# Kernel optimization log

Hardware: AMD Instinct MI355X
Metric: run time of the kernel (lower is better)

## Reference

```python
import jax, jax.numpy as jnp
import numpy as np

M_GROUP = 8  # VENOM m: pattern period along in_features

def _nm_mask(in_features, dtype):
    # NMVectorSparsifier.get_random_mask keeps positions 0 and 2 of every group of m=8
    pat = jnp.array([1.0, 0.0, 1.0, 0.0, 0.0, 0.0, 0.0, 0.0], dtype=dtype)
    return jnp.tile(pat, in_features // M_GROUP)  # [in_features]


def setup_inputs() -> dict:
    key = jax.random.key(0)
    k1, k2, k3 = jax.random.split(key, 3)
    B, S, D_IN, D_OUT = 8, 2048, 4096, 4096
    x = jax.random.normal(k1, (B, S, D_IN), dtype=jnp.float32)
    weight = jax.random.normal(k2, (D_OUT, D_IN), dtype=jnp.float32) * 0.02
    bias = jax.random.normal(k3, (D_OUT,), dtype=jnp.float32) * 0.02
    return {"x": x, "weight": weight, "bias": bias}


def reference(x, weight, bias):
    # y = x @ (W * mask)^T + b  -- N:M (2:8) vector-sparse linear, dense-math reference
    mask = _nm_mask(weight.shape[1], weight.dtype)  # [D_IN]
    w = weight * mask[None, :]                      # [D_OUT, D_IN]
    return jnp.einsum('bsd,od->bso', x, w) + bias
```

## Files before the change

### kernel.cpp

```cpp
#include <hip/hip_runtime.h>
#include <hip/hip_bf16.h>
#include <stdint.h>

#define MROWS 16384
#define DIN   4096
#define DOUT  4096
#define KEFF  1024

typedef __attribute__((ext_vector_type(8))) __bf16 bf16x8;
typedef __attribute__((ext_vector_type(4))) float f32x4;

#define AS1 __attribute__((address_space(1)))
#define AS3 __attribute__((address_space(3)))

__device__ __forceinline__ uint32_t f2bf_rne(float f) {
  union { float f; uint32_t u; } v; v.f = f;
  uint32_t u = v.u;
  return (u + 0x7fffu + ((u >> 16) & 1u)) >> 16;
}

__global__ void venom_gather_all(const float* __restrict__ x,
                                 const float* __restrict__ w,
                                 uint2* __restrict__ xg, uint2* __restrict__ wg) {
  const int PX = MROWS * (DIN / 16);
  const int PW = DOUT * (DIN / 16);
  int stride = gridDim.x * blockDim.x;
  for (int i = blockIdx.x * blockDim.x + threadIdx.x; i < PX + PW; i += stride) {
    const float* src; uint2* dst; int idx;
    if (i < PX) { src = x; dst = xg; idx = i; }
    else        { src = w; dst = wg; idx = i - PX; }
    const float4* p = reinterpret_cast<const float4*>(src) + (size_t)idx * 4;
    float4 a = p[0];
    float4 b = p[2];
    uint2 r;
    r.x = f2bf_rne(a.x) | (f2bf_rne(a.z) << 16);
    r.y = f2bf_rne(b.x) | (f2bf_rne(b.z) << 16);
    dst[idx] = r;
  }
}

#define BM 256
#define BN 256
#define BK 64
#define NT (KEFF / BK)
#define TPB 4
#define LTOT (NT * TPB)

__device__ __forceinline__ int swz_off(int R, int lg) {
  int sr = R >> 1;
  return sr * 128 + (((((R & 1) << 2) | lg) ^ (sr & 7)) << 4);
}

#define WAIT_VM(n) asm volatile("s_waitcnt vmcnt(" #n ")" ::: "memory")
#define BAR() __builtin_amdgcn_s_barrier()

__global__ __launch_bounds__(512, 2) void venom_gemm_p3(
    const __bf16* __restrict__ A, const __bf16* __restrict__ Bm,
    const float* __restrict__ bias, float* __restrict__ C) {
  __shared__ __bf16 As[2][2][128 * 64];
  __shared__ __bf16 Bs[2][2][128 * 64];

  int nwg = gridDim.x;
  int cpx = nwg >> 3;
  int bid = blockIdx.x;
  int swz = (bid & 7) * cpx + (bid >> 3);
  int mblk = swz >> 2;
  int ngrp = swz & 3;

  int t = threadIdx.x;
  int wid = t >> 6, l = t & 63;
  int wr = wid >> 2, wc = wid & 3;
  int lr = l & 15, lg = l >> 4;

  const __bf16* Ag = A + (size_t)(mblk * BM) * KEFF;

  float biasr[TPB][4];
  #pragma unroll
  for (int j = 0; j < TPB; ++j)
    #pragma unroll
    for (int ni = 0; ni < 4; ++ni)
      biasr[j][ni] = bias[(ngrp * TPB + j) * BN + wc * 64 + ni * 16 + lr];

  f32x4 acc[8][4] = {};

  auto stage_half = [&](int L2, int kh) {
    const int buf = L2 & 1;
    const int j2 = L2 >> 4;
    const int kt2 = L2 & (NT - 1);
    const __bf16* Bg = Bm + (size_t)((ngrp * TPB + j2) * BN) * KEFF;
    const int k0 = kt2 * BK + kh * 32;
    #pragma unroll
    for (int i = 0; i < 2; ++i) {
      int e = i * 512 + t;
      int sr = e >> 3;
      int s = (e & 7) ^ (sr & 7);
      int row = sr * 2 + (s >> 2);
      int koff = (s & 3) * 8;
      __builtin_amdgcn_global_load_lds(
          (const AS1 uint32_t*)(Ag + (size_t)row * KEFF + k0 + koff),
          ((AS3 uint32_t*)&As[buf][kh][0]) + e * 4, 16, 0, 0);
      __builtin_amdgcn_global_load_lds(
          (const AS1 uint32_t*)(Bg + (size_t)row * KEFF + k0 + koff),
          ((AS3 uint32_t*)&Bs[buf][kh][0]) + e * 4, 16, 0, 0);
    }
  };

  stage_half(0, 0);
  stage_half(0, 1);
  stage_half(1, 0);
  WAIT_VM(8);
  BAR();

  bf16x8 bfrag[4];

  #pragma unroll
  for (int j = 0; j < TPB; ++j) {
    #pragma unroll 1
    for (int kt = 0; kt < NT; ++kt) {
      const int L = j * NT + kt;
      const int cur = kt & 1;

      #pragma unroll
      for (int ph = 0; ph < 4; ++ph) {
        const int mh = ph & 1, kh = ph >> 1;
        const char* aB = (const char*)&As[cur][kh][0];
        bf16x8 af[4];
        #pragma unroll
        for (int mi = 0; mi < 4; ++mi)
          af[mi] = *(const bf16x8*)(aB + swz_off(wr * 128 + mh * 64 + mi * 16 + lr, lg));
        if (mh == 0) {
          const char* bB = (const char*)&Bs[cur][kh][0];
          #pragma unroll
          for (int ni = 0; ni < 4; ++ni)
            bfrag[ni] = *(const bf16x8*)(bB + swz_off(wc * 64 + ni * 16 + lr, lg));
          if (kh == 0) { if (L + 1 < LTOT) stage_half(L + 1, 1); }
          else         { if (L + 2 < LTOT) stage_half(L + 2, 0); }
        }

        BAR();
        __builtin_amdgcn_s_setprio(1);
        #pragma unroll
        for (int mi = 0; mi < 4; ++mi)
          #pragma unroll
          for (int ni = 0; ni < 4; ++ni)
            acc[mh * 4 + mi][ni] = __builtin_amdgcn_mfma_f32_16x16x32_bf16(
                af[mi], bfrag[ni], acc[mh * 4 + mi][ni], 0, 0, 0);
        __builtin_amdgcn_s_setprio(0);

        if (ph == 1) {
          if (L <= LTOT - 2) WAIT_VM(8);
          else               WAIT_VM(0);
          BAR();
        } else if (ph == 3) {
          if (L <= LTOT - 3)      WAIT_VM(8);
          else if (L == LTOT - 2) WAIT_VM(4);
          else                    WAIT_VM(0);
          BAR();
        } else {
          BAR();
        }
      }
    }

    {
      int colbase = (ngrp * TPB + j) * BN + wc * 64;
      int rowbase = mblk * BM + wr * 128;
      #pragma unroll
      for (int mh = 0; mh < 2; ++mh)
        #pragma unroll
        for (int mi = 0; mi < 4; ++mi) {
          int row0 = rowbase + mh * 64 + mi * 16 + lg * 4;
          #pragma unroll
          for (int ni = 0; ni < 4; ++ni) {
            int col = colbase + ni * 16 + lr;
            f32x4 cv = acc[mh * 4 + mi][ni];
            #pragma unroll
            for (int jj = 0; jj < 4; ++jj)
              C[(size_t)(row0 + jj) * DOUT + col] = cv[jj] + biasr[j][ni];
          }
        }
      #pragma unroll
      for (int q = 0; q < 8; ++q)
        #pragma unroll
        for (int ni = 0; ni < 4; ++ni)
          acc[q][ni] = (f32x4){0.f, 0.f, 0.f, 0.f};
    }
  }
}

__global__ void venom_naive(const float* __restrict__ x, const float* __restrict__ w,
                            const float* __restrict__ bias, float* __restrict__ out) {
  size_t total = (size_t)MROWS * DOUT;
  size_t stride = (size_t)gridDim.x * blockDim.x;
  for (size_t idx = (size_t)blockIdx.x * blockDim.x + threadIdx.x; idx < total;
       idx += stride) {
    int m = (int)(idx / DOUT), n = (int)(idx % DOUT);
    const float* xr = x + (size_t)m * DIN;
    const float* wr = w + (size_t)n * DIN;
    float s = 0.f;
    for (int g = 0; g < DIN / 8; ++g)
      s += xr[g * 8] * wr[g * 8] + xr[g * 8 + 2] * wr[g * 8 + 2];
    out[idx] = s + bias[n];
  }
}

extern "C" void kernel_launch(void* const* d_in, const int* in_sizes, int n_in,
                              void* d_out, int out_size, void* d_ws, size_t ws_size,
                              hipStream_t stream) {
  const float* x    = (const float*)d_in[0];
  const float* wgt  = (const float*)d_in[1];
  const float* bias = (const float*)d_in[2];
  float* out = (float*)d_out;

  const size_t xg_bytes = (size_t)MROWS * KEFF * 2;
  const size_t wg_bytes = (size_t)DOUT * KEFF * 2;

  if (ws_size < xg_bytes + wg_bytes) {
    venom_naive<<<2048, 256, 0, stream>>>(x, wgt, bias, out);
    return;
  }

  uint32_t* xg = (uint32_t*)d_ws;
  uint32_t* wg = (uint32_t*)((char*)d_ws + xg_bytes);

  venom_gather_all<<<2048, 256, 0, stream>>>(x, wgt, (uint2*)xg, (uint2*)wg);

  venom_gemm_p3<<<(MROWS / BM) * (DOUT / BN / TPB), 512, 0, stream>>>(
      (const __bf16*)xg, (const __bf16*)wg, bias, out);
}
```

Before: 287.0 us.

## Switch GEMM to 32x32x16 MFMA tiles and restructure prefetch pipeline

New measurement: 293.3 us. 1.02x slower.

```diff
diff --git a/kernel.cpp b/kernel.cpp
--- a/kernel.cpp
+++ b/kernel.cpp
@@ -7,8 +7,8 @@
 #define DOUT  4096
 #define KEFF  1024
 
-typedef __attribute__((ext_vector_type(8))) __bf16 bf16x8;
-typedef __attribute__((ext_vector_type(4))) float f32x4;
+typedef __attribute__((ext_vector_type(8)))  __bf16 bf16x8;
+typedef __attribute__((ext_vector_type(16))) float  f32x16;
 
 #define AS1 __attribute__((address_space(1)))
 #define AS3 __attribute__((address_space(3)))
@@ -46,15 +46,15 @@
 #define TPB 4
 #define LTOT (NT * TPB)
 
-__device__ __forceinline__ int swz_off(int R, int lg) {
+__device__ __forceinline__ int swz_off(int R, int slot) {
   int sr = R >> 1;
-  return sr * 128 + (((((R & 1) << 2) | lg) ^ (sr & 7)) << 4);
+  return sr * 128 + (((((R & 1) << 2) | slot) ^ (sr & 7)) << 4);
 }
 
 #define WAIT_VM(n) asm volatile("s_waitcnt vmcnt(" #n ")" ::: "memory")
 #define BAR() __builtin_amdgcn_s_barrier()
 
-__global__ __launch_bounds__(512, 2) void venom_gemm_p3(
+__global__ __launch_bounds__(512, 2) void venom_gemm_w32(
     const __bf16* __restrict__ A, const __bf16* __restrict__ Bm,
     const float* __restrict__ bias, float* __restrict__ C) {
   __shared__ __bf16 As[2][2][128 * 64];
@@ -70,25 +70,22 @@
   int t = threadIdx.x;
   int wid = t >> 6, l = t & 63;
   int wr = wid >> 2, wc = wid & 3;
-  int lr = l & 15, lg = l >> 4;
+  int lc = l & 31, hi = l >> 5;
 
   const __bf16* Ag = A + (size_t)(mblk * BM) * KEFF;
 
-  float biasr[TPB][4];
+  float biasr[TPB][2];
   #pragma unroll
   for (int j = 0; j < TPB; ++j)
     #pragma unroll
-    for (int ni = 0; ni < 4; ++ni)
-      biasr[j][ni] = bias[(ngrp * TPB + j) * BN + wc * 64 + ni * 16 + lr];
-
-  f32x4 acc[8][4] = {};
-
-  auto stage_half = [&](int L2, int kh) {
+    for (int tj = 0; tj < 2; ++tj)
+      biasr[j][tj] = bias[(ngrp * TPB + j) * BN + wc * 64 + tj * 32 + lc];
+
+  f32x16 acc[4][2] = {};
+
+  auto stageA = [&](int L2, int kh) {
     const int buf = L2 & 1;
-    const int j2 = L2 >> 4;
-    const int kt2 = L2 & (NT - 1);
-    const __bf16* Bg = Bm + (size_t)((ngrp * TPB + j2) * BN) * KEFF;
-    const int k0 = kt2 * BK + kh * 32;
+    const int k0 = (L2 & (NT - 1)) * BK + kh * 32;
     #pragma unroll
     for (int i = 0; i < 2; ++i) {
       int e = i * 512 + t;
@@ -99,19 +96,31 @@
       __builtin_amdgcn_global_load_lds(
           (const AS1 uint32_t*)(Ag + (size_t)row * KEFF + k0 + koff),
           ((AS3 uint32_t*)&As[buf][kh][0]) + e * 4, 16, 0, 0);
+    }
+  };
+  auto stageB = [&](int L2, int kh) {
+    const int buf = L2 & 1;
+    const __bf16* Bg = Bm + (size_t)((ngrp * TPB + (L2 >> 4)) * BN) * KEFF;
+    const int k0 = (L2 & (NT - 1)) * BK + kh * 32;
+    #pragma unroll
+    for (int i = 0; i < 2; ++i) {
+      int e = i * 512 + t;
+      int sr = e >> 3;
+      int s = (e & 7) ^ (sr & 7);
+      int row = sr * 2 + (s >> 2);
+      int koff = (s & 3) * 8;
       __builtin_amdgcn_global_load_lds(
           (const AS1 uint32_t*)(Bg + (size_t)row * KEFF + k0 + koff),
           ((AS3 uint32_t*)&Bs[buf][kh][0]) + e * 4, 16, 0, 0);
     }
   };
 
-  stage_half(0, 0);
-  stage_half(0, 1);
-  stage_half(1, 0);
-  WAIT_VM(8);
-  BAR();
-
-  bf16x8 bfrag[4];
+  stageA(0, 0);
+  stageB(0, 0);
+  stageA(0, 1);
+  stageB(0, 1);
+
+  bf16x8 bfr[2][2];
 
   #pragma unroll
   for (int j = 0; j < TPB; ++j) {
@@ -119,46 +128,52 @@
     for (int kt = 0; kt < NT; ++kt) {
       const int L = j * NT + kt;
       const int cur = kt & 1;
+      const bool last = (L == LTOT - 1);
 
       #pragma unroll
       for (int ph = 0; ph < 4; ++ph) {
         const int mh = ph & 1, kh = ph >> 1;
+
+        if (ph == 0) WAIT_VM(4);
+        if (ph == 2) { if (last) WAIT_VM(0); else WAIT_VM(4); }
+        BAR();
+
         const char* aB = (const char*)&As[cur][kh][0];
-        bf16x8 af[4];
+        bf16x8 af[2][2];
         #pragma unroll
-        for (int mi = 0; mi < 4; ++mi)
-          af[mi] = *(const bf16x8*)(aB + swz_off(wr * 128 + mh * 64 + mi * 16 + lr, lg));
+        for (int mt = 0; mt < 2; ++mt)
+          #pragma unroll
+          for (int ks = 0; ks < 2; ++ks)
+            af[mt][ks] = *(const bf16x8*)(aB +
+                swz_off(wr * 128 + mh * 64 + mt * 32 + lc, ks * 2 + hi));
         if (mh == 0) {
           const char* bB = (const char*)&Bs[cur][kh][0];
           #pragma unroll
-          for (int ni = 0; ni < 4; ++ni)
-            bfrag[ni] = *(const bf16x8*)(bB + swz_off(wc * 64 + ni * 16 + lr, lg));
-          if (kh == 0) { if (L + 1 < LTOT) stage_half(L + 1, 1); }
-          else         { if (L + 2 < LTOT) stage_half(L + 2, 0); }
+          for (int nt = 0; nt < 2; ++nt)
+            #pragma unroll
+            for (int ks = 0; ks < 2; ++ks)
+              bfr[nt][ks] = *(const bf16x8*)(bB +
+                  swz_off(wc * 64 + nt * 32 + lc, ks * 2 + hi));
         }
 
-        BAR();
+        if (!last) {
+          if (ph == 0) stageA(L + 1, 0);
+          else if (ph == 1) stageB(L + 1, 0);
+          else if (ph == 2) stageA(L + 1, 1);
+          else stageB(L + 1, 1);
+        }
+
         __builtin_amdgcn_s_setprio(1);
         #pragma unroll
-        for (int mi = 0; mi < 4; ++mi)
-          #pragma unroll
-          for (int ni = 0; ni < 4; ++ni)
-            acc[mh * 4 + mi][ni] = __builtin_amdgcn_mfma_f32_16x16x32_bf16(
-                af[mi], bfrag[ni], acc[mh * 4 + mi][ni], 0, 0, 0);
+        for (int mt = 0; mt < 2; ++mt)
+          #pragma unroll
+          for (int nt = 0; nt < 2; ++nt) {
+            acc[mh * 2 + mt][nt] = __builtin_amdgcn_mfma_f32_32x32x16_bf16(
+                af[mt][0], bfr[nt][0], acc[mh * 2 + mt][nt], 0, 0, 0);
+            acc[mh * 2 + mt][nt] = __builtin_amdgcn_mfma_f32_32x32x16_bf16(
+                af[mt][1], bfr[nt][1], acc[mh * 2 + mt][nt], 0, 0, 0);
+          }
         __builtin_amdgcn_s_setprio(0);
-
-        if (ph == 1) {
-          if (L <= LTOT - 2) WAIT_VM(8);
-          else               WAIT_VM(0);
-          BAR();
-        } else if (ph == 3) {
-          if (L <= LTOT - 3)      WAIT_VM(8);
-          else if (L == LTOT - 2) WAIT_VM(4);
-          else                    WAIT_VM(0);
-          BAR();
-        } else {
-          BAR();
-        }
       }
     }
 
@@ -166,24 +181,19 @@
       int colbase = (ngrp * TPB + j) * BN + wc * 64;
       int rowbase = mblk * BM + wr * 128;
       #pragma unroll
-      for (int mh = 0; mh < 2; ++mh)
+      for (int ti = 0; ti < 4; ++ti)
         #pragma unroll
-        for (int mi = 0; mi < 4; ++mi) {
-          int row0 = rowbase + mh * 64 + mi * 16 + lg * 4;
-          #pragma unroll
-          for (int ni = 0; ni < 4; ++ni) {
-            int col = colbase + ni * 16 + lr;
-            f32x4 cv = acc[mh * 4 + mi][ni];
-            #pragma unroll
-            for (int jj = 0; jj < 4; ++jj)
-              C[(size_t)(row0 + jj) * DOUT + col] = cv[jj] + biasr[j][ni];
+        for (int tj = 0; tj < 2; ++tj) {
+          int col = colbase + tj * 32 + lc;
+          float bv = biasr[j][tj];
+          f32x16 cv = acc[ti][tj];
+          #pragma unroll
+          for (int r = 0; r < 16; ++r) {
+            int row = rowbase + ti * 32 + (r & 3) + 8 * (r >> 2) + 4 * hi;
+            C[(size_t)row * DOUT + col] = cv[r] + bv;
           }
+          acc[ti][tj] = (f32x16){};
         }
-      #pragma unroll
-      for (int q = 0; q < 8; ++q)
-        #pragma unroll
-        for (int ni = 0; ni < 4; ++ni)
-          acc[q][ni] = (f32x4){0.f, 0.f, 0.f, 0.f};
     }
   }
 }
@@ -225,6 +235,6 @@
 
   venom_gather_all<<<2048, 256, 0, stream>>>(x, wgt, (uint2*)xg, (uint2*)wg);
 
-  venom_gemm_p3<<<(MROWS / BM) * (DOUT / BN / TPB), 512, 0, stream>>>(
+  venom_gemm_w32<<<(MROWS / BM) * (DOUT / BN / TPB), 512, 0, stream>>>(
       (const __bf16*)xg, (const __bf16*)wg, bias, out);
 }
```

## Shrink GEMM tiles to 128x128 and iterate M tiles per block over a fixed N slice

Applied to the files above, without the earlier changes.

New measurement: 304.9 us. 1.06x slower.

```diff
diff --git a/kernel.cpp b/kernel.cpp
--- a/kernel.cpp
+++ b/kernel.cpp
@@ -39,11 +39,11 @@
   }
 }
 
-#define BM 256
-#define BN 256
+#define BM 128
+#define BN 128
 #define BK 64
 #define NT (KEFF / BK)
-#define TPB 4
+#define TPB 8
 #define LTOT (NT * TPB)
 
 __device__ __forceinline__ int swz_off(int R, int lg) {
@@ -54,44 +54,40 @@
 #define WAIT_VM(n) asm volatile("s_waitcnt vmcnt(" #n ")" ::: "memory")
 #define BAR() __builtin_amdgcn_s_barrier()
 
-__global__ __launch_bounds__(512, 2) void venom_gemm_p3(
+__global__ __launch_bounds__(256, 2) void venom_gemm_2c(
     const __bf16* __restrict__ A, const __bf16* __restrict__ Bm,
     const float* __restrict__ bias, float* __restrict__ C) {
-  __shared__ __bf16 As[2][2][128 * 64];
-  __shared__ __bf16 Bs[2][2][128 * 64];
+  __shared__ __bf16 As[2][2][128 * 32];
+  __shared__ __bf16 Bs[2][2][128 * 32];
 
   int nwg = gridDim.x;
   int cpx = nwg >> 3;
   int bid = blockIdx.x;
   int swz = (bid & 7) * cpx + (bid >> 3);
-  int mblk = swz >> 2;
-  int ngrp = swz & 3;
+  int nblk = swz & 31;
+  int mgrp = swz >> 5;
 
   int t = threadIdx.x;
   int wid = t >> 6, l = t & 63;
-  int wr = wid >> 2, wc = wid & 3;
+  int wr = wid >> 1, wc = wid & 1;
   int lr = l & 15, lg = l >> 4;
 
-  const __bf16* Ag = A + (size_t)(mblk * BM) * KEFF;
-
-  float biasr[TPB][4];
+  const __bf16* Bg = Bm + (size_t)(nblk * BN) * KEFF;
+
+  float biasr[4];
   #pragma unroll
-  for (int j = 0; j < TPB; ++j)
-    #pragma unroll
-    for (int ni = 0; ni < 4; ++ni)
-      biasr[j][ni] = bias[(ngrp * TPB + j) * BN + wc * 64 + ni * 16 + lr];
-
-  f32x4 acc[8][4] = {};
+  for (int ni = 0; ni < 4; ++ni)
+    biasr[ni] = bias[nblk * BN + wc * 64 + ni * 16 + lr];
+
+  f32x4 acc[4][4] = {};
 
   auto stage_half = [&](int L2, int kh) {
     const int buf = L2 & 1;
-    const int j2 = L2 >> 4;
-    const int kt2 = L2 & (NT - 1);
-    const __bf16* Bg = Bm + (size_t)((ngrp * TPB + j2) * BN) * KEFF;
-    const int k0 = kt2 * BK + kh * 32;
+    const int k0 = (L2 & (NT - 1)) * BK + kh * 32;
+    const __bf16* Ag = A + (size_t)((mgrp * TPB + (L2 >> 4)) * BM) * KEFF;
     #pragma unroll
     for (int i = 0; i < 2; ++i) {
-      int e = i * 512 + t;
+      int e = i * 256 + t;
       int sr = e >> 3;
       int s = (e & 7) ^ (sr & 7);
       int row = sr * 2 + (s >> 2);
@@ -107,83 +103,79 @@
 
   stage_half(0, 0);
   stage_half(0, 1);
-  stage_half(1, 0);
-  WAIT_VM(8);
-  BAR();
-
-  bf16x8 bfrag[4];
-
-  #pragma unroll
+
+  #pragma unroll 1
   for (int j = 0; j < TPB; ++j) {
     #pragma unroll 1
     for (int kt = 0; kt < NT; ++kt) {
       const int L = j * NT + kt;
-      const int cur = kt & 1;
-
-      #pragma unroll
-      for (int ph = 0; ph < 4; ++ph) {
-        const int mh = ph & 1, kh = ph >> 1;
-        const char* aB = (const char*)&As[cur][kh][0];
-        bf16x8 af[4];
-        #pragma unroll
-        for (int mi = 0; mi < 4; ++mi)
-          af[mi] = *(const bf16x8*)(aB + swz_off(wr * 128 + mh * 64 + mi * 16 + lr, lg));
-        if (mh == 0) {
-          const char* bB = (const char*)&Bs[cur][kh][0];
+      const int cur = L & 1;
+      const bool more = (L + 1 < LTOT);
+
+      WAIT_VM(4);
+      BAR();
+      {
+        const char* aB = (const char*)&As[cur][0][0];
+        const char* bB = (const char*)&Bs[cur][0][0];
+        bf16x8 af[4], bf[4];
+        #pragma unroll
+        for (int mi = 0; mi < 4; ++mi)
+          af[mi] = *(const bf16x8*)(aB + swz_off(wr * 64 + mi * 16 + lr, lg));
+        #pragma unroll
+        for (int ni = 0; ni < 4; ++ni)
+          bf[ni] = *(const bf16x8*)(bB + swz_off(wc * 64 + ni * 16 + lr, lg));
+        if (more) stage_half(L + 1, 0);
+        __builtin_amdgcn_s_setprio(1);
+        #pragma unroll
+        for (int mi = 0; mi < 4; ++mi)
           #pragma unroll
           for (int ni = 0; ni < 4; ++ni)
-            bfrag[ni] = *(const bf16x8*)(bB + swz_off(wc * 64 + ni * 16 + lr, lg));
-          if (kh == 0) { if (L + 1 < LTOT) stage_half(L + 1, 1); }
-          else         { if (L + 2 < LTOT) stage_half(L + 2, 0); }
-        }
-
-        BAR();
+            acc[mi][ni] = __builtin_amdgcn_mfma_f32_16x16x32_bf16(
+                af[mi], bf[ni], acc[mi][ni], 0, 0, 0);
+        __builtin_amdgcn_s_setprio(0);
+      }
+
+      if (more) WAIT_VM(4);
+      else      WAIT_VM(0);
+      BAR();
+      {
+        const char* aB = (const char*)&As[cur][1][0];
+        const char* bB = (const char*)&Bs[cur][1][0];
+        bf16x8 af[4], bf[4];
+        #pragma unroll
+        for (int mi = 0; mi < 4; ++mi)
+          af[mi] = *(const bf16x8*)(aB + swz_off(wr * 64 + mi * 16 + lr, lg));
+        #pragma unroll
+        for (int ni = 0; ni < 4; ++ni)
+          bf[ni] = *(const bf16x8*)(bB + swz_off(wc * 64 + ni * 16 + lr, lg));
+        if (more) stage_half(L + 1, 1);
         __builtin_amdgcn_s_setprio(1);
         #pragma unroll
         for (int mi = 0; mi < 4; ++mi)
           #pragma unroll
           for (int ni = 0; ni < 4; ++ni)
-            acc[mh * 4 + mi][ni] = __builtin_amdgcn_mfma_f32_16x16x32_bf16(
-                af[mi], bfrag[ni], acc[mh * 4 + mi][ni], 0, 0, 0);
+            acc[mi][ni] = __builtin_amdgcn_mfma_f32_16x16x32_bf16(
+                af[mi], bf[ni], acc[mi][ni], 0, 0, 0);
         __builtin_amdgcn_s_setprio(0);
-
-        if (ph == 1) {
-          if (L <= LTOT - 2) WAIT_VM(8);
-          else               WAIT_VM(0);
-          BAR();
-        } else if (ph == 3) {
-          if (L <= LTOT - 3)      WAIT_VM(8);
-          else if (L == LTOT - 2) WAIT_VM(4);
-          else                    WAIT_VM(0);
-          BAR();
-        } else {
-          BAR();
+      }
+    }
+
+    {
+      int colbase = nblk * BN + wc * 64;
+      int rowbase = (mgrp * TPB + j) * BM + wr * 64;
+      #pragma unroll
+      for (int mi = 0; mi < 4; ++mi) {
+        int row0 = rowbase + mi * 16 + lg * 4;
+        #pragma unroll
+        for (int ni = 0; ni < 4; ++ni) {
+          int col = colbase + ni * 16 + lr;
+          f32x4 cv = acc[mi][ni];
+          #pragma unroll
+          for (int jj = 0; jj < 4; ++jj)
+            C[(size_t)(row0 + jj) * DOUT + col] = cv[jj] + biasr[ni];
+          acc[mi][ni] = (f32x4){0.f, 0.f, 0.f, 0.f};
         }
       }
-    }
-
-    {
-      int colbase = (ngrp * TPB + j) * BN + wc * 64;
-      int rowbase = mblk * BM + wr * 128;
-      #pragma unroll
-      for (int mh = 0; mh < 2; ++mh)
-        #pragma unroll
-        for (int mi = 0; mi < 4; ++mi) {
-          int row0 = rowbase + mh * 64 + mi * 16 + lg * 4;
-          #pragma unroll
-          for (int ni = 0; ni < 4; ++ni) {
-            int col = colbase + ni * 16 + lr;
-            f32x4 cv = acc[mh * 4 + mi][ni];
-            #pragma unroll
-            for (int jj = 0; jj < 4; ++jj)
-              C[(size_t)(row0 + jj) * DOUT + col] = cv[jj] + biasr[j][ni];
-          }
-        }
-      #pragma unroll
-      for (int q = 0; q < 8; ++q)
-        #pragma unroll
-        for (int ni = 0; ni < 4; ++ni)
-          acc[q][ni] = (f32x4){0.f, 0.f, 0.f, 0.f};
     }
   }
 }
@@ -225,6 +217,6 @@
 
   venom_gather_all<<<2048, 256, 0, stream>>>(x, wgt, (uint2*)xg, (uint2*)wg);
 
-  venom_gemm_p3<<<(MROWS / BM) * (DOUT / BN / TPB), 512, 0, stream>>>(
+  venom_gemm_2c<<<(MROWS / BM / TPB) * (DOUT / BN), 256, 0, stream>>>(
       (const __bf16*)xg, (const __bf16*)wg, bias, out);
 }
```
